# Kernel optimization log

Measured on AMD Instinct MI355X. Metric: run time of the kernel, lower is better.

Reference implementation:

```python
import jax, jax.numpy as jnp
import numpy as np

N_USER, N_ITEM, D = 50000, 30000, 64
N = N_USER + N_ITEM
NNZ_UI, NNZ_R, NNZ_II = 1000000, 800000, 300000
IMG_F, TXT_F = 512, 384
EPS = 1e-5


def spmm(rows, cols, vals, x, n_out):
    # sparse [n_out, n_in] @ dense [n_in, d] via gather + segment-sum
    return jax.ops.segment_sum(vals[:, None] * x[cols], rows, num_segments=n_out)


def leaky_relu(x):
    return jnp.where(x >= 0, x, 0.01 * x)


def setup_inputs() -> dict:
    key = jax.random.key(0)
    ks = jax.random.split(key, 32)
    f = lambda i, shape, s=0.05: (jax.random.normal(ks[i], shape, dtype=jnp.float32) * s)
    inp = {
        'user_emb': f(0, (N_USER, D)),
        'item_emb': f(1, (N_ITEM, D)),
        'image_embedding': f(2, (N_ITEM, IMG_F), 1.0),
        'text_embedding': f(3, (N_ITEM, TXT_F), 1.0),
        'W_img': f(4, (IMG_F, D)), 'b_img': jnp.zeros((D,), jnp.float32),
        'bn_g_img': jnp.ones((D,), jnp.float32), 'bn_b_img': jnp.zeros((D,), jnp.float32),
        'W_txt': f(5, (TXT_F, D)), 'b_txt': jnp.zeros((D,), jnp.float32),
        'bn_g_txt': jnp.ones((D,), jnp.float32), 'bn_b_txt': jnp.zeros((D,), jnp.float32),
        'W_gate_img': f(6, (D, D)), 'b_gate_img': jnp.zeros((D,), jnp.float32),
        'W_gate_txt': f(7, (D, D)), 'b_gate_txt': jnp.zeros((D,), jnp.float32),
        'W_common1': f(8, (D, D)), 'b_common1': jnp.zeros((D,), jnp.float32),
        'w_common2': f(9, (D,)),
        'ui_vals': jax.random.uniform(ks[10], (NNZ_UI,), dtype=jnp.float32),
        'R_vals': jax.random.uniform(ks[11], (NNZ_R,), dtype=jnp.float32),
        'ii_img_vals': jax.random.uniform(ks[12], (NNZ_II,), dtype=jnp.float32),
        'ii_txt_vals': jax.random.uniform(ks[13], (NNZ_II,), dtype=jnp.float32),
        'ui_rows': jax.random.randint(ks[14], (NNZ_UI,), 0, N, dtype=jnp.int32),
        'ui_cols': jax.random.randint(ks[15], (NNZ_UI,), 0, N, dtype=jnp.int32),
        'R_rows': jax.random.randint(ks[16], (NNZ_R,), 0, N_USER, dtype=jnp.int32),
        'R_cols': jax.random.randint(ks[17], (NNZ_R,), 0, N_ITEM, dtype=jnp.int32),
        'ii_img_rows': jax.random.randint(ks[18], (NNZ_II,), 0, N_ITEM, dtype=jnp.int32),
        'ii_img_cols': jax.random.randint(ks[19], (NNZ_II,), 0, N_ITEM, dtype=jnp.int32),
        'ii_txt_rows': jax.random.randint(ks[20], (NNZ_II,), 0, N_ITEM, dtype=jnp.int32),
        'ii_txt_cols': jax.random.randint(ks[21], (NNZ_II,), 0, N_ITEM, dtype=jnp.int32),
    }
    return inp


def reference(user_emb, item_emb, image_embedding, text_embedding,
              W_img, b_img, bn_g_img, bn_b_img,
              W_txt, b_txt, bn_g_txt, bn_b_txt,
              W_gate_img, b_gate_img, W_gate_txt, b_gate_txt,
              W_common1, b_common1, w_common2,
              ui_vals, R_vals, ii_img_vals, ii_txt_vals,
              ui_rows, ui_cols, R_rows, R_cols,
              ii_img_rows, ii_img_cols, ii_txt_rows, ii_txt_cols):
    # ---- user_item_GCN: adj = original + diffusion (fused edge list) ----
    cat = jnp.concatenate([item_emb, user_emb], axis=0)  # [N, D], item first per source
    embs = [cat]
    for _ in range(2):
        cat = spmm(ui_rows, ui_cols, ui_vals, cat, N)
        embs.append(cat)
    content_embedding = jnp.stack(embs, axis=1).mean(axis=1)  # [N, D]

    # ---- modal projections (BN inference, dropout=eval identity) ----
    def project(x, W, b, g, beta):
        h = x @ W + b
        h = h * (g / jnp.sqrt(1.0 + EPS)) + beta  # BatchNorm1d, running stats (0, 1)
        return leaky_relu(h)

    img_feat = project(image_embedding, W_img, b_img, bn_g_img, bn_b_img)  # [I, D]
    txt_feat = project(text_embedding, W_txt, b_txt, bn_g_txt, bn_b_txt)

    # ---- item_item_GCN ----
    def modal_branch(feat, Wg, bg, rows, cols, vals):
        it = item_emb * jax.nn.sigmoid(feat @ Wg + bg)  # gated item embedding
        for _ in range(2):
            it = spmm(rows, cols, vals, it, N_ITEM)
        us = spmm(R_rows, R_cols, R_vals, it, N_USER)  # R @ item -> user
        return jnp.concatenate([us, it], axis=0)  # [N, D], user first per source

    image_ui = modal_branch(img_feat, W_gate_img, b_gate_img, ii_img_rows, ii_img_cols, ii_img_vals)
    text_ui = modal_branch(txt_feat, W_gate_txt, b_gate_txt, ii_txt_rows, ii_txt_cols, ii_txt_vals)

    # ---- gate_attention_fusion (non-tiktok: 2 modalities) ----
    def att_score(e):
        return leaky_relu(e @ W_common1 + b_common1) @ w_common2  # [N]

    att = jnp.stack([att_score(image_ui), att_score(text_ui)], axis=-1)  # [N, 2]
    w = jax.nn.softmax(att, axis=-1)
    common = w[:, 0:1] * image_ui + w[:, 1:2] * text_ui
    special_img = image_ui - common
    special_txt = text_ui - common

    return jnp.stack([content_embedding, special_img, special_txt, common], axis=0)  # [4, N, D]
```

## Files before the change

kernel.cpp:

```cpp
#include <hip/hip_runtime.h>

#define N_USER 50000
#define N_ITEM 30000
#define DIM    64
#define NTOT   80000
#define NNZ_UI 1000000
#define NNZ_R  800000
#define NNZ_II 300000
#define IMG_F  512
#define TXT_F  384

#define NROWS_ALL 190000
#define NNZ_ALL   2400000
#define BASE_R    NTOT
#define BASE_II   (NTOT + N_USER)
#define BASE_IT   (NTOT + N_USER + N_ITEM)

#define RB_BITS   9
#define RB_ROWS   512
#define NBUCK     ((NROWS_ALL + RB_ROWS - 1) / RB_ROWS)
#define NBLK_A2   400
#define EDG_A2    6000

#define NBLK_PG   625
#define NBLK_UIP  5000
#define NBLK_I16  1875
#define NBLK_U16  3125
#define NBLK_CP   1875

#define NBLK_M1   (2 * NBLK_PG + NBLK_UIP)
#define NBLK_M2   (NBLK_UIP + 2 * NBLK_I16)
#define NBLK_RC   (NBLK_U16 + 2 * NBLK_CP)

__device__ __forceinline__ int edge_row(int i,
        const int* __restrict__ r0, const int* __restrict__ r1,
        const int* __restrict__ r2, const int* __restrict__ r3){
    if (i < NNZ_UI)                       return r0[i];
    if (i < NNZ_UI + NNZ_R)               return BASE_R  + r1[i - NNZ_UI];
    if (i < NNZ_UI + NNZ_R + NNZ_II)      return BASE_II + r2[i - NNZ_UI - NNZ_R];
    return BASE_IT + r3[i - NNZ_UI - NNZ_R - NNZ_II];
}

__device__ __forceinline__ void edge_all(int i,
        const int* __restrict__ r0, const int* __restrict__ c0, const float* __restrict__ v0,
        const int* __restrict__ r1, const int* __restrict__ c1, const float* __restrict__ v1,
        const int* __restrict__ r2, const int* __restrict__ c2, const float* __restrict__ v2,
        const int* __restrict__ r3, const int* __restrict__ c3, const float* __restrict__ v3,
        int& gr, int& col, float& val){
    if (i < NNZ_UI){
        gr = r0[i]; col = c0[i]; val = v0[i];
    } else if (i < NNZ_UI + NNZ_R){
        int j = i - NNZ_UI;               gr = BASE_R  + r1[j]; col = c1[j]; val = v1[j];
    } else if (i < NNZ_UI + NNZ_R + NNZ_II){
        int j = i - NNZ_UI - NNZ_R;       gr = BASE_II + r2[j]; col = c2[j]; val = v2[j];
    } else {
        int j = i - NNZ_UI - NNZ_R - NNZ_II; gr = BASE_IT + r3[j]; col = c3[j]; val = v3[j];
    }
}

__global__ __launch_bounds__(256) void k_bhist(const int* __restrict__ r0,
        const int* __restrict__ r1, const int* __restrict__ r2,
        const int* __restrict__ r3, int* __restrict__ bcnt){
    __shared__ int h[NBUCK];
    for (int i = threadIdx.x; i < NBUCK; i += 256) h[i] = 0;
    __syncthreads();
    const int stride = gridDim.x * 256;
    for (int i = blockIdx.x * 256 + threadIdx.x; i < NNZ_ALL; i += stride){
        int gr = edge_row(i, r0, r1, r2, r3);
        atomicAdd(&h[gr >> RB_BITS], 1);
    }
    __syncthreads();
    for (int i = threadIdx.x; i < NBUCK; i += 256){
        int c = h[i];
        if (c) atomicAdd(&bcnt[i], c);
    }
}

__global__ __launch_bounds__(512) void k_bscan(const int* __restrict__ bcnt,
        int* __restrict__ bbase, int* __restrict__ off){
    __shared__ int sh[512];
    const int t = threadIdx.x;
    int v = (t < NBUCK) ? bcnt[t] : 0;
    sh[t] = v;
    __syncthreads();
    for (int d = 1; d < 512; d <<= 1){
        int u = (t >= d) ? sh[t - d] : 0;
        __syncthreads();
        sh[t] += u;
        __syncthreads();
    }
    if (t < NBUCK) bbase[t] = sh[t] - v;
    if (t == NBUCK - 1){
        bbase[NBUCK] = sh[t];
        off[NROWS_ALL] = sh[t];
    }
}

__global__ __launch_bounds__(256) void k_bin(
        const int* __restrict__ r0, const int* __restrict__ c0, const float* __restrict__ v0,
        const int* __restrict__ r1, const int* __restrict__ c1, const float* __restrict__ v1,
        const int* __restrict__ r2, const int* __restrict__ c2, const float* __restrict__ v2,
        const int* __restrict__ r3, const int* __restrict__ c3, const float* __restrict__ v3,
        const int* __restrict__ bbase, int* __restrict__ bcur,
        int2* __restrict__ binned){
    __shared__ int lofs[NBUCK];
    __shared__ int lcur[NBUCK];
    const int t = threadIdx.x;
    for (int i = t; i < NBUCK; i += 256){ lofs[i] = 0; lcur[i] = 0; }
    __syncthreads();
    const int s0 = blockIdx.x * EDG_A2, s1 = s0 + EDG_A2;
    for (int i = s0 + t; i < s1; i += 256){
        int gr = edge_row(i, r0, r1, r2, r3);
        atomicAdd(&lofs[gr >> RB_BITS], 1);
    }
    __syncthreads();
    for (int i = t; i < NBUCK; i += 256){
        int c = lofs[i];
        lofs[i] = c ? (bbase[i] + atomicAdd(&bcur[i], c)) : 0;
    }
    __syncthreads();
    for (int i = s0 + t; i < s1; i += 256){
        int gr, col; float val;
        edge_all(i, r0, c0, v0, r1, c1, v1, r2, c2, v2, r3, c3, v3, gr, col, val);
        int b = gr >> RB_BITS;
        int slot = atomicAdd(&lcur[b], 1);
        binned[lofs[b] + slot] = make_int2((col << RB_BITS) | (gr & (RB_ROWS - 1)),
                                           __float_as_int(val));
    }
}

__global__ __launch_bounds__(256) void k_scatter(const int* __restrict__ bbase,
        const int2* __restrict__ binned, int* __restrict__ off,
        int2* __restrict__ csr){
    __shared__ int h[RB_ROWS];
    const int t = threadIdx.x;
    const int b = blockIdx.x;
    const int base = bbase[b];
    const int nb = bbase[b + 1] - base;
    h[t] = 0; h[t + 256] = 0;
    __syncthreads();
    for (int i = t; i < nb; i += 256)
        atomicAdd(&h[binned[base + i].x & (RB_ROWS - 1)], 1);
    __syncthreads();
    if (t < 64){
        int v[8], s = 0;
#pragma unroll
        for (int k = 0; k < 8; ++k){ v[k] = h[t * 8 + k]; s += v[k]; }
        int incl = s;
#pragma unroll
        for (int d = 1; d < 64; d <<= 1){
            int u = __shfl_up(incl, d, 64);
            if (t >= d) incl += u;
        }
        int run = incl - s;
#pragma unroll
        for (int k = 0; k < 8; ++k){ int tmp = v[k]; h[t * 8 + k] = run; run += tmp; }
    }
    __syncthreads();
    const int row0 = b << RB_BITS;
    for (int i = t; i < RB_ROWS; i += 256){
        int r = row0 + i;
        if (r < NROWS_ALL) off[r] = base + h[i];
    }
    __syncthreads();
    for (int i = t; i < nb; i += 256){
        int2 rec = binned[base + i];
        int lr = rec.x & (RB_ROWS - 1);
        int slot = atomicAdd(&h[lr], 1);
        csr[base + slot] = make_int2(rec.x >> RB_BITS, rec.y);
    }
}

__device__ __forceinline__ const float* cat_row(int c,
        const float* __restrict__ item, const float* __restrict__ user){
    return (c < N_ITEM) ? (item + ((long)c << 6)) : (user + ((long)(c - N_ITEM) << 6));
}

__device__ __forceinline__ void fma4(float4& a, float v, const float4& x){
    a.x = fmaf(v, x.x, a.x);
    a.y = fmaf(v, x.y, a.y);
    a.z = fmaf(v, x.z, a.z);
    a.w = fmaf(v, x.w, a.w);
}

__device__ __forceinline__ void pull_body(const int* __restrict__ off,
        const int2* __restrict__ csr, const float* __restrict__ x,
        float* __restrict__ y, int r, int l){
    int s = off[r], e = off[r + 1];
    float4 a0 = {0.f,0.f,0.f,0.f}, a1 = {0.f,0.f,0.f,0.f};
    float4 a2 = {0.f,0.f,0.f,0.f}, a3 = {0.f,0.f,0.f,0.f};
    int j = s;
    for (; j + 4 <= e; j += 4){
        int2 e0 = csr[j], e1 = csr[j+1], e2 = csr[j+2], e3 = csr[j+3];
        const float4 x0 = *reinterpret_cast<const float4*>(x + ((long)e0.x << 6) + l);
        const float4 x1 = *reinterpret_cast<const float4*>(x + ((long)e1.x << 6) + l);
        const float4 x2 = *reinterpret_cast<const float4*>(x + ((long)e2.x << 6) + l);
        const float4 x3 = *reinterpret_cast<const float4*>(x + ((long)e3.x << 6) + l);
        fma4(a0, __int_as_float(e0.y), x0);
        fma4(a1, __int_as_float(e1.y), x1);
        fma4(a2, __int_as_float(e2.y), x2);
        fma4(a3, __int_as_float(e3.y), x3);
    }
    for (; j < e; ++j){
        int2 e0 = csr[j];
        const float4 x0 = *reinterpret_cast<const float4*>(x + ((long)e0.x << 6) + l);
        fma4(a0, __int_as_float(e0.y), x0);
    }
    a0.x = (a0.x + a1.x) + (a2.x + a3.x);
    a0.y = (a0.y + a1.y) + (a2.y + a3.y);
    a0.z = (a0.z + a1.z) + (a2.z + a3.z);
    a0.w = (a0.w + a1.w) + (a2.w + a3.w);
    *reinterpret_cast<float4*>(y + ((long)r << 6) + l) = a0;
}

__device__ __forceinline__ void pull_cat_body(const int* __restrict__ off,
        const int2* __restrict__ csr, const float* __restrict__ item,
        const float* __restrict__ user, float* __restrict__ y, int r, int l){
    int s = off[r], e = off[r + 1];
    float4 a0 = {0.f,0.f,0.f,0.f}, a1 = {0.f,0.f,0.f,0.f};
    float4 a2 = {0.f,0.f,0.f,0.f}, a3 = {0.f,0.f,0.f,0.f};
    int j = s;
    for (; j + 4 <= e; j += 4){
        int2 e0 = csr[j], e1 = csr[j+1], e2 = csr[j+2], e3 = csr[j+3];
        const float4 x0 = *reinterpret_cast<const float4*>(cat_row(e0.x, item, user) + l);
        const float4 x1 = *reinterpret_cast<const float4*>(cat_row(e1.x, item, user) + l);
        const float4 x2 = *reinterpret_cast<const float4*>(cat_row(e2.x, item, user) + l);
        const float4 x3 = *reinterpret_cast<const float4*>(cat_row(e3.x, item, user) + l);
        fma4(a0, __int_as_float(e0.y), x0);
        fma4(a1, __int_as_float(e1.y), x1);
        fma4(a2, __int_as_float(e2.y), x2);
        fma4(a3, __int_as_float(e3.y), x3);
    }
    for (; j < e; ++j){
        int2 e0 = csr[j];
        const float4 x0 = *reinterpret_cast<const float4*>(cat_row(e0.x, item, user) + l);
        fma4(a0, __int_as_float(e0.y), x0);
    }
    a0.x = (a0.x + a1.x) + (a2.x + a3.x);
    a0.y = (a0.y + a1.y) + (a2.y + a3.y);
    a0.z = (a0.z + a1.z) + (a2.z + a3.z);
    a0.w = (a0.w + a1.w) + (a2.w + a3.w);
    *reinterpret_cast<float4*>(y + ((long)r << 6) + l) = a0;
}

__device__ __forceinline__ void pull_mean_body(const int* __restrict__ off,
        const int2* __restrict__ csr, const float* __restrict__ x,
        const float* __restrict__ item, const float* __restrict__ user,
        float* __restrict__ o0, int r, int l){
    int s = off[r], e = off[r + 1];
    float4 a0 = {0.f,0.f,0.f,0.f}, a1 = {0.f,0.f,0.f,0.f};
    float4 a2 = {0.f,0.f,0.f,0.f}, a3 = {0.f,0.f,0.f,0.f};
    int j = s;
    for (; j + 4 <= e; j += 4){
        int2 e0 = csr[j], e1 = csr[j+1], e2 = csr[j+2], e3 = csr[j+3];
        const float4 x0 = *reinterpret_cast<const float4*>(x + ((long)e0.x << 6) + l);
        const float4 x1 = *reinterpret_cast<const float4*>(x + ((long)e1.x << 6) + l);
        const float4 x2 = *reinterpret_cast<const float4*>(x + ((long)e2.x << 6) + l);
        const float4 x3 = *reinterpret_cast<const float4*>(x + ((long)e3.x << 6) + l);
        fma4(a0, __int_as_float(e0.y), x0);
        fma4(a1, __int_as_float(e1.y), x1);
        fma4(a2, __int_as_float(e2.y), x2);
        fma4(a3, __int_as_float(e3.y), x3);
    }
    for (; j < e; ++j){
        int2 e0 = csr[j];
        const float4 x0 = *reinterpret_cast<const float4*>(x + ((long)e0.x << 6) + l);
        fma4(a0, __int_as_float(e0.y), x0);
    }
    a0.x = (a0.x + a1.x) + (a2.x + a3.x);
    a0.y = (a0.y + a1.y) + (a2.y + a3.y);
    a0.z = (a0.z + a1.z) + (a2.z + a3.z);
    a0.w = (a0.w + a1.w) + (a2.w + a3.w);
    const float4 av = *reinterpret_cast<const float4*>(cat_row(r, item, user) + l);
    const float4 xv = *reinterpret_cast<const float4*>(x + ((long)r << 6) + l);
    float4 o;
    o.x = (av.x + xv.x + a0.x) * (1.0f / 3.0f);
    o.y = (av.y + xv.y + a0.y) * (1.0f / 3.0f);
    o.z = (av.z + xv.z + a0.z) * (1.0f / 3.0f);
    o.w = (av.w + xv.w + a0.w) * (1.0f / 3.0f);
    *reinterpret_cast<float4*>(o0 + ((long)r << 6) + l) = o;
}

__global__ void k_pull2(const int* __restrict__ offA, const int2* __restrict__ csr,
                        const float* __restrict__ xA, float* __restrict__ yA,
                        const int* __restrict__ offB, const float* __restrict__ xB,
                        float* __restrict__ yB, int nrows, int nblk_half){
    int b = blockIdx.x;
    const int* off; const float* x; float* y;
    if (b < nblk_half){ off = offA; x = xA; y = yA; }
    else              { b -= nblk_half; off = offB; x = xB; y = yB; }
    int t = b * 256 + threadIdx.x;
    int r = t >> 4;
    if (r >= nrows) return;
    pull_body(off, csr, x, y, r, (t & 15) << 2);
}

__global__ __launch_bounds__(256) void k_mega1(
        const int* __restrict__ offUI, const int2* __restrict__ csr,
        const float* __restrict__ user,
        float* __restrict__ hop1out,
        const float* __restrict__ Xi, const float* __restrict__ Wi,
        const float* __restrict__ bi, const float* __restrict__ gi,
        const float* __restrict__ bei, const float* __restrict__ Wgi,
        const float* __restrict__ bgi,
        const float* __restrict__ Xt, const float* __restrict__ Wt,
        const float* __restrict__ bt, const float* __restrict__ gt,
        const float* __restrict__ bet, const float* __restrict__ Wgt,
        const float* __restrict__ bgt,
        const float* __restrict__ item,
        float* __restrict__ Pi, float* __restrict__ Pt){
    __shared__ float xs[48][36];
    __shared__ float ws[32][64];

    if (blockIdx.x >= 2 * NBLK_PG){
        int pb = blockIdx.x - 2 * NBLK_PG;
        int t = pb * 256 + threadIdx.x;
        int r = t >> 4;
        pull_cat_body(offUI, csr, item, user, hop1out, r, (t & 15) << 2);
        return;
    }

    const int t  = threadIdx.x;
    const int tr = t >> 4;
    const int tc = t & 15;
    const int pgb = blockIdx.x;
    const bool isTxt = pgb >= NBLK_PG;
    const int  blk   = isTxt ? (pgb - NBLK_PG) : pgb;
    const int  K     = isTxt ? TXT_F : IMG_F;
    const float* X   = isTxt ? Xt  : Xi;
    const float* W   = isTxt ? Wt  : Wi;
    const float* bb  = isTxt ? bt  : bi;
    const float* gg  = isTxt ? gt  : gi;
    const float* be  = isTxt ? bet : bei;
    const float* Wg  = isTxt ? Wgt : Wgi;
    const float* bg  = isTxt ? bgt : bgi;
    float* outP      = isTxt ? Pt  : Pi;
    const int row0   = blk * 48;

    float acc[3][4];
#pragma unroll
    for (int i = 0; i < 3; ++i)
#pragma unroll
        for (int j = 0; j < 4; ++j) acc[i][j] = 0.f;

    for (int ks = 0; ks < K; ks += 32){
        __syncthreads();
        {
            int row = t >> 3, col = (t & 7) << 2;
            *reinterpret_cast<float4*>(&xs[row][col]) =
                *reinterpret_cast<const float4*>(X + (long)(row0 + row) * K + ks + col);
            int f = t + 256;
            if (f < 384){
                row = f >> 3; col = (f & 7) << 2;
                *reinterpret_cast<float4*>(&xs[row][col]) =
                    *reinterpret_cast<const float4*>(X + (long)(row0 + row) * K + ks + col);
            }
        }
        {
            const float4* wsrc = reinterpret_cast<const float4*>(W + (long)ks * 64);
            float4* wdst = reinterpret_cast<float4*>(&ws[0][0]);
            wdst[t]       = wsrc[t];
            wdst[t + 256] = wsrc[t + 256];
        }
        __syncthreads();
#pragma unroll 8
        for (int kk = 0; kk < 32; kk += 2){
            float2 a[3];
#pragma unroll
            for (int i = 0; i < 3; ++i)
                a[i] = *reinterpret_cast<const float2*>(&xs[tr + 16 * i][kk]);
            float4 b0 = *reinterpret_cast<const float4*>(&ws[kk][tc * 4]);
            float4 b1 = *reinterpret_cast<const float4*>(&ws[kk + 1][tc * 4]);
#pragma unroll
            for (int i = 0; i < 3; ++i){
                acc[i][0] = fmaf(a[i].x, b0.x, acc[i][0]);
                acc[i][1] = fmaf(a[i].x, b0.y, acc[i][1]);
                acc[i][2] = fmaf(a[i].x, b0.z, acc[i][2]);
                acc[i][3] = fmaf(a[i].x, b0.w, acc[i][3]);
                acc[i][0] = fmaf(a[i].y, b1.x, acc[i][0]);
                acc[i][1] = fmaf(a[i].y, b1.y, acc[i][1]);
                acc[i][2] = fmaf(a[i].y, b1.z, acc[i][2]);
                acc[i][3] = fmaf(a[i].y, b1.w, acc[i][3]);
            }
        }
    }

    const float4 b4  = reinterpret_cast<const float4*>(bb)[tc];
    const float4 g4  = reinterpret_cast<const float4*>(gg)[tc];
    const float4 be4 = reinterpret_cast<const float4*>(be)[tc];
    float4 h[3];
#pragma unroll
    for (int i = 0; i < 3; ++i){
        h[i].x = (acc[i][0] + b4.x) * (g4.x * 0.99999500003749943f) + be4.x;
        h[i].y = (acc[i][1] + b4.y) * (g4.y * 0.99999500003749943f) + be4.y;
        h[i].z = (acc[i][2] + b4.z) * (g4.z * 0.99999500003749943f) + be4.z;
        h[i].w = (acc[i][3] + b4.w) * (g4.w * 0.99999500003749943f) + be4.w;
        h[i].x = (h[i].x >= 0.f) ? h[i].x : 0.01f * h[i].x;
        h[i].y = (h[i].y >= 0.f) ? h[i].y : 0.01f * h[i].y;
        h[i].z = (h[i].z >= 0.f) ? h[i].z : 0.01f * h[i].z;
        h[i].w = (h[i].w >= 0.f) ? h[i].w : 0.01f * h[i].w;
    }

    float ac2[3][4];
#pragma unroll
    for (int i = 0; i < 3; ++i)
#pragma unroll
        for (int j = 0; j < 4; ++j) ac2[i][j] = 0.f;

#pragma unroll
    for (int ph = 0; ph < 2; ++ph){
        __syncthreads();
        if ((tc >> 3) == ph){
            int lc = (tc & 7) << 2;
#pragma unroll
            for (int i = 0; i < 3; ++i)
                *reinterpret_cast<float4*>(&xs[tr + 16 * i][lc]) = h[i];
        }
        {
            const float4* wsrc = reinterpret_cast<const float4*>(Wg) + ph * 512;
            float4* wdst = reinterpret_cast<float4*>(&ws[0][0]);
            wdst[t]       = wsrc[t];
            wdst[t + 256] = wsrc[t + 256];
        }
        __syncthreads();
#pragma unroll 8
        for (int kk = 0; kk < 32; kk += 2){
            float2 a[3];
#pragma unroll
            for (int i = 0; i < 3; ++i)
                a[i] = *reinterpret_cast<const float2*>(&xs[tr + 16 * i][kk]);
            float4 b0 = *reinterpret_cast<const float4*>(&ws[kk][tc * 4]);
            float4 b1 = *reinterpret_cast<const float4*>(&ws[kk + 1][tc * 4]);
#pragma unroll
            for (int i = 0; i < 3; ++i){
                ac2[i][0] = fmaf(a[i].x, b0.x, ac2[i][0]);
                ac2[i][1] = fmaf(a[i].x, b0.y, ac2[i][1]);
                ac2[i][2] = fmaf(a[i].x, b0.z, ac2[i][2]);
                ac2[i][3] = fmaf(a[i].x, b0.w, ac2[i][3]);
                ac2[i][0] = fmaf(a[i].y, b1.x, ac2[i][0]);
                ac2[i][1] = fmaf(a[i].y, b1.y, ac2[i][1]);
                ac2[i][2] = fmaf(a[i].y, b1.z, ac2[i][2]);
                ac2[i][3] = fmaf(a[i].y, b1.w, ac2[i][3]);
            }
        }
    }

    const float4 bg4 = reinterpret_cast<const float4*>(bg)[tc];
#pragma unroll
    for (int i = 0; i < 3; ++i){
        int r = tr + 16 * i;
        const float4 iv = *reinterpret_cast<const float4*>(
                item + (long)(row0 + r) * 64 + tc * 4);
        float4 o;
        o.x = iv.x / (1.f + __expf(-(ac2[i][0] + bg4.x)));
        o.y = iv.y / (1.f + __expf(-(ac2[i][1] + bg4.y)));
        o.z = iv.z / (1.f + __expf(-(ac2[i][2] + bg4.z)));
        o.w = iv.w / (1.f + __expf(-(ac2[i][3] + bg4.w)));
        *reinterpret_cast<float4*>(outP + (long)(row0 + r) * 64 + tc * 4) = o;
    }
}

__global__ void k_mega2c(const int* __restrict__ offUI, const int2* __restrict__ csr,
        const float* __restrict__ hop1,
        const float* __restrict__ item, const float* __restrict__ user,
        float* __restrict__ o0,
        const int* __restrict__ offI2, const float* __restrict__ P_img,
        float* __restrict__ Q_img,
        const int* __restrict__ offT2, const float* __restrict__ P_txt,
        float* __restrict__ Q_txt){
    const int tid = threadIdx.x;
    if (blockIdx.x < NBLK_UIP){
        int t = blockIdx.x * 256 + tid;
        int r = t >> 4;
        pull_mean_body(offUI, csr, hop1, item, user, o0, r, (t & 15) << 2);
    } else {
        int m = blockIdx.x - NBLK_UIP;
        const int* off; const float* x; float* y;
        if (m < NBLK_I16){ off = offI2; x = P_img; y = Q_img; }
        else             { m -= NBLK_I16; off = offT2; x = P_txt; y = Q_txt; }
        int t = m * 256 + tid;
        int r = t >> 4;
        pull_body(off, csr, x, y, r, (t & 15) << 2);
    }
}

__global__ void k_pullRC(const int* __restrict__ off, const int2* __restrict__ csr,
                         const float* __restrict__ xA, float* __restrict__ yA,
                         const float* __restrict__ xB, float* __restrict__ yB,
                         float* __restrict__ dA, float* __restrict__ dB){
    int bid = blockIdx.x;
    const int tid = threadIdx.x;
    if (bid >= NBLK_U16){
        int c = bid - NBLK_U16;
        const float4* src; float4* dst;
        if (c < NBLK_CP){ src = reinterpret_cast<const float4*>(xA);
                          dst = reinterpret_cast<float4*>(dA); }
        else { c -= NBLK_CP; src = reinterpret_cast<const float4*>(xB);
               dst = reinterpret_cast<float4*>(dB); }
        int i = c * 256 + tid;
        dst[i] = src[i];
        return;
    }
    int t = bid * 256 + tid;
    int r = t >> 4;
    int l = (t & 15) << 2;
    int s = off[r], e = off[r + 1];
    float4 pA0 = {0.f,0.f,0.f,0.f}, pA1 = {0.f,0.f,0.f,0.f};
    float4 pB0 = {0.f,0.f,0.f,0.f}, pB1 = {0.f,0.f,0.f,0.f};
    int j = s;
    for (; j + 2 <= e; j += 2){
        int2 e0 = csr[j];
        int2 e1 = csr[j + 1];
        float v0 = __int_as_float(e0.y);
        float v1 = __int_as_float(e1.y);
        long o0 = ((long)e0.x << 6) + l;
        long o1 = ((long)e1.x << 6) + l;
        const float4 xa0 = *reinterpret_cast<const float4*>(xA + o0);
        const float4 xa1 = *reinterpret_cast<const float4*>(xA + o1);
        const float4 xb0 = *reinterpret_cast<const float4*>(xB + o0);
        const float4 xb1 = *reinterpret_cast<const float4*>(xB + o1);
        fma4(pA0, v0, xa0);
        fma4(pA1, v1, xa1);
        fma4(pB0, v0, xb0);
        fma4(pB1, v1, xb1);
    }
    if (j < e){
        int2 e0 = csr[j];
        float v0 = __int_as_float(e0.y);
        long o0 = ((long)e0.x << 6) + l;
        const float4 xa0 = *reinterpret_cast<const float4*>(xA + o0);
        const float4 xb0 = *reinterpret_cast<const float4*>(xB + o0);
        fma4(pA0, v0, xa0);
        fma4(pB0, v0, xb0);
    }
    pA0.x += pA1.x; pA0.y += pA1.y; pA0.z += pA1.z; pA0.w += pA1.w;
    pB0.x += pB1.x; pB0.y += pB1.y; pB0.z += pB1.z; pB0.w += pB1.w;
    *reinterpret_cast<float4*>(yA + ((long)r << 6) + l) = pA0;
    *reinterpret_cast<float4*>(yB + ((long)r << 6) + l) = pB0;
}

__global__ __launch_bounds__(256) void k_fuse(const float* __restrict__ img,
        const float* __restrict__ txt, const float* __restrict__ W1,
        const float* __restrict__ b1, const float* __restrict__ w2,
        float* __restrict__ out){
    __shared__ float si[64][68];
    __shared__ float st[64][68];
    __shared__ float w1s[64][64];
    const int t  = threadIdx.x;
    const int tr = t >> 4;
    const int tc = t & 15;
    const long row0 = (long)blockIdx.x * 64;

#pragma unroll
    for (int i = 0; i < 4; ++i){
        int r = tr + 16 * i;
        *reinterpret_cast<float4*>(&si[r][tc * 4]) =
            *reinterpret_cast<const float4*>(img + (row0 + r) * 64 + tc * 4);
        *reinterpret_cast<float4*>(&st[r][tc * 4]) =
            *reinterpret_cast<const float4*>(txt + (row0 + r) * 64 + tc * 4);
    }
    {
        const float4* wsrc = reinterpret_cast<const float4*>(W1);
        float4* wdst = reinterpret_cast<float4*>(&w1s[0][0]);
#pragma unroll
        for (int i = 0; i < 4; ++i) wdst[t + 256 * i] = wsrc[t + 256 * i];
    }
    __syncthreads();

    float ai[4][4], at[4][4];
#pragma unroll
    for (int i = 0; i < 4; ++i)
#pragma unroll
        for (int j = 0; j < 4; ++j){ ai[i][j] = 0.f; at[i][j] = 0.f; }

#pragma unroll 8
    for (int kk = 0; kk < 64; kk += 2){
        float4 b0 = *reinterpret_cast<const float4*>(&w1s[kk][tc * 4]);
        float4 b1v = *reinterpret_cast<const float4*>(&w1s[kk + 1][tc * 4]);
#pragma unroll
        for (int i = 0; i < 4; ++i){
            float2 a = *reinterpret_cast<const float2*>(&si[tr + 16 * i][kk]);
            float2 c = *reinterpret_cast<const float2*>(&st[tr + 16 * i][kk]);
            ai[i][0] = fmaf(a.x, b0.x, ai[i][0]);
            ai[i][1] = fmaf(a.x, b0.y, ai[i][1]);
            ai[i][2] = fmaf(a.x, b0.z, ai[i][2]);
            ai[i][3] = fmaf(a.x, b0.w, ai[i][3]);
            ai[i][0] = fmaf(a.y, b1v.x, ai[i][0]);
            ai[i][1] = fmaf(a.y, b1v.y, ai[i][1]);
            ai[i][2] = fmaf(a.y, b1v.z, ai[i][2]);
            ai[i][3] = fmaf(a.y, b1v.w, ai[i][3]);
            at[i][0] = fmaf(c.x, b0.x, at[i][0]);
            at[i][1] = fmaf(c.x, b0.y, at[i][1]);
            at[i][2] = fmaf(c.x, b0.z, at[i][2]);
            at[i][3] = fmaf(c.x, b0.w, at[i][3]);
            at[i][0] = fmaf(c.y, b1v.x, at[i][0]);
            at[i][1] = fmaf(c.y, b1v.y, at[i][1]);
            at[i][2] = fmaf(c.y, b1v.z, at[i][2]);
            at[i][3] = fmaf(c.y, b1v.w, at[i][3]);
        }
    }

    const float4 b14 = reinterpret_cast<const float4*>(b1)[tc];
    const float4 w24 = reinterpret_cast<const float4*>(w2)[tc];
    float pi[4], pt[4];
#pragma unroll
    for (int i = 0; i < 4; ++i){
        float hi0 = ai[i][0] + b14.x; hi0 = (hi0 >= 0.f) ? hi0 : 0.01f * hi0;
        float hi1 = ai[i][1] + b14.y; hi1 = (hi1 >= 0.f) ? hi1 : 0.01f * hi1;
        float hi2 = ai[i][2] + b14.z; hi2 = (hi2 >= 0.f) ? hi2 : 0.01f * hi2;
        float hi3 = ai[i][3] + b14.w; hi3 = (hi3 >= 0.f) ? hi3 : 0.01f * hi3;
        float ht0 = at[i][0] + b14.x; ht0 = (ht0 >= 0.f) ? ht0 : 0.01f * ht0;
        float ht1 = at[i][1] + b14.y; ht1 = (ht1 >= 0.f) ? ht1 : 0.01f * ht1;
        float ht2 = at[i][2] + b14.z; ht2 = (ht2 >= 0.f) ? ht2 : 0.01f * ht2;
        float ht3 = at[i][3] + b14.w; ht3 = (ht3 >= 0.f) ? ht3 : 0.01f * ht3;
        pi[i] = fmaf(hi0, w24.x, fmaf(hi1, w24.y, fmaf(hi2, w24.z, hi3 * w24.w)));
        pt[i] = fmaf(ht0, w24.x, fmaf(ht1, w24.y, fmaf(ht2, w24.z, ht3 * w24.w)));
    }
#pragma unroll
    for (int m = 1; m < 16; m <<= 1){
#pragma unroll
        for (int i = 0; i < 4; ++i){
            pi[i] += __shfl_xor(pi[i], m, 64);
            pt[i] += __shfl_xor(pt[i], m, 64);
        }
    }

    const long NTD = (long)NTOT * DIM;
#pragma unroll
    for (int i = 0; i < 4; ++i){
        int r = tr + 16 * i;
        float mx = fmaxf(pi[i], pt[i]);
        float ei = __expf(pi[i] - mx), et = __expf(pt[i] - mx);
        float inv = 1.f / (ei + et);
        float wi = ei * inv, wt = et * inv;
        const float4 ie = *reinterpret_cast<const float4*>(&si[r][tc * 4]);
        const float4 te = *reinterpret_cast<const float4*>(&st[r][tc * 4]);
        float4 cm, oi, ot;
        cm.x = wi * ie.x + wt * te.x;
        cm.y = wi * ie.y + wt * te.y;
        cm.z = wi * ie.z + wt * te.z;
        cm.w = wi * ie.w + wt * te.w;
        oi.x = ie.x - cm.x; oi.y = ie.y - cm.y; oi.z = ie.z - cm.z; oi.w = ie.w - cm.w;
        ot.x = te.x - cm.x; ot.y = te.y - cm.y; ot.z = te.z - cm.z; ot.w = te.w - cm.w;
        long o = (row0 + r) * 64 + tc * 4;
        *reinterpret_cast<float4*>(out + NTD + o)     = oi;
        *reinterpret_cast<float4*>(out + 2 * NTD + o) = ot;
        *reinterpret_cast<float4*>(out + 3 * NTD + o) = cm;
    }
}

extern "C" void kernel_launch(void* const* d_in, const int* in_sizes, int n_in,
                              void* d_out, int out_size, void* d_ws, size_t ws_size,
                              hipStream_t stream){
    const float* user_emb  = (const float*)d_in[0];
    const float* item_emb  = (const float*)d_in[1];
    const float* image_emb = (const float*)d_in[2];
    const float* text_emb  = (const float*)d_in[3];
    const float* W_img = (const float*)d_in[4];
    const float* b_img = (const float*)d_in[5];
    const float* g_img = (const float*)d_in[6];
    const float* be_img= (const float*)d_in[7];
    const float* W_txt = (const float*)d_in[8];
    const float* b_txt = (const float*)d_in[9];
    const float* g_txt = (const float*)d_in[10];
    const float* be_txt= (const float*)d_in[11];
    const float* W_gi  = (const float*)d_in[12];
    const float* b_gi  = (const float*)d_in[13];
    const float* W_gt  = (const float*)d_in[14];
    const float* b_gt  = (const float*)d_in[15];
    const float* W_c1  = (const float*)d_in[16];
    const float* b_c1  = (const float*)d_in[17];
    const float* w_c2  = (const float*)d_in[18];
    const float* ui_vals = (const float*)d_in[19];
    const float* R_vals  = (const float*)d_in[20];
    const float* ii_iv   = (const float*)d_in[21];
    const float* ii_tv   = (const float*)d_in[22];
    const int* ui_rows = (const int*)d_in[23];
    const int* ui_cols = (const int*)d_in[24];
    const int* R_rows  = (const int*)d_in[25];
    const int* R_cols  = (const int*)d_in[26];
    const int* ii_ir   = (const int*)d_in[27];
    const int* ii_ic   = (const int*)d_in[28];
    const int* ii_tr   = (const int*)d_in[29];
    const int* ii_tc   = (const int*)d_in[30];

    const long ND = (long)NTOT * DIM;
    const long ID = (long)N_ITEM * DIM;
    const long UD = (long)N_USER * DIM;

    float* out = (float*)d_out;
    float* o0 = out;
    float* o1 = out + ND;
    float* o2 = out + 2 * ND;
    float* o3 = out + 3 * ND;

    float* P_img = o3;
    float* P_txt = o3 + ID;
    float* Q_img = o1;
    float* Q_txt = o1 + ID;
    float* H_img = o3;
    float* H_txt = o3 + ID;

    int2* binned = (int2*)o0;

    int2* csr   = (int2*)d_ws;
    int*  off   = (int*)(csr + NNZ_ALL);
    int*  bcnt  = off + NROWS_ALL + 4;
    int*  bcur  = bcnt + NBUCK;
    int*  bbase = bcur + NBUCK;

    hipMemsetAsync(bcnt, 0, 2 * NBUCK * sizeof(int), stream);
    k_bhist<<<512, 256, 0, stream>>>(ui_rows, R_rows, ii_ir, ii_tr, bcnt);
    k_bscan<<<1, 512, 0, stream>>>(bcnt, bbase, off);
    k_bin<<<NBLK_A2, 256, 0, stream>>>(
        ui_rows, ui_cols, ui_vals,  R_rows, R_cols, R_vals,
        ii_ir, ii_ic, ii_iv,        ii_tr, ii_tc, ii_tv,
        bbase, bcur, binned);
    k_scatter<<<NBUCK, 256, 0, stream>>>(bbase, binned, off, csr);

    const int* offUI = off;
    const int* offR  = off + BASE_R;
    const int* offI2 = off + BASE_II;
    const int* offT2 = off + BASE_IT;

    k_mega1<<<NBLK_M1, 256, 0, stream>>>(
        offUI, csr, user_emb, o2,
        image_emb, W_img, b_img, g_img, be_img, W_gi, b_gi,
        text_emb,  W_txt, b_txt, g_txt, be_txt, W_gt, b_gt,
        item_emb, P_img, P_txt);

    k_mega2c<<<NBLK_M2, 256, 0, stream>>>(
        offUI, csr, o2, item_emb, user_emb, o0,
        offI2, P_img, Q_img, offT2, P_txt, Q_txt);

    k_pull2<<<2 * NBLK_I16, 256, 0, stream>>>(
        offI2, csr, Q_img, H_img, offT2, Q_txt, H_txt, N_ITEM, NBLK_I16);

    k_pullRC<<<NBLK_RC, 256, 0, stream>>>(
        offR, csr, H_img, o1, H_txt, o2, o1 + UD, o2 + UD);

    k_fuse<<<NTOT / 64, 256, 0, stream>>>(o1, o2, W_c1, b_c1, w_c2, out);
}
```

Before: 562.5 us.

## Fuse histogram, scan and binning into one cooperative kernel; widen projection K-tile

Merges the bucket histogram, the prefix scan and the binning pass into a single cooperative kernel. It reuses the per-block local histogram that binning already computes, separates the phases with grid-wide syncs, and does the scan with a wavefront shuffle. This removes two kernel launches and a second full read of the row arrays. Separately, the projection GEMM in k_mega1 now uses a 64-wide K tile, and the gate GEMM runs in one 64-deep pass instead of two 32-deep phases, which halves the number of block barriers. The cost is larger shared-memory use per block, which may lower occupancy, plus the overhead of grid sync and a requirement that all 400 blocks be co-resident.

```diff
diff --git a/kernel.cpp b/kernel.cpp
--- a/kernel.cpp
+++ b/kernel.cpp
@@ -1,4 +1,7 @@
 #include <hip/hip_runtime.h>
+#include <hip/hip_cooperative_groups.h>
+
+namespace cg = cooperative_groups;
 
 #define N_USER 50000
 #define N_ITEM 30000
@@ -58,51 +61,13 @@
     }
 }
 
-__global__ __launch_bounds__(256) void k_bhist(const int* __restrict__ r0,
-        const int* __restrict__ r1, const int* __restrict__ r2,
-        const int* __restrict__ r3, int* __restrict__ bcnt){
-    __shared__ int h[NBUCK];
-    for (int i = threadIdx.x; i < NBUCK; i += 256) h[i] = 0;
-    __syncthreads();
-    const int stride = gridDim.x * 256;
-    for (int i = blockIdx.x * 256 + threadIdx.x; i < NNZ_ALL; i += stride){
-        int gr = edge_row(i, r0, r1, r2, r3);
-        atomicAdd(&h[gr >> RB_BITS], 1);
-    }
-    __syncthreads();
-    for (int i = threadIdx.x; i < NBUCK; i += 256){
-        int c = h[i];
-        if (c) atomicAdd(&bcnt[i], c);
-    }
-}
-
-__global__ __launch_bounds__(512) void k_bscan(const int* __restrict__ bcnt,
-        int* __restrict__ bbase, int* __restrict__ off){
-    __shared__ int sh[512];
-    const int t = threadIdx.x;
-    int v = (t < NBUCK) ? bcnt[t] : 0;
-    sh[t] = v;
-    __syncthreads();
-    for (int d = 1; d < 512; d <<= 1){
-        int u = (t >= d) ? sh[t - d] : 0;
-        __syncthreads();
-        sh[t] += u;
-        __syncthreads();
-    }
-    if (t < NBUCK) bbase[t] = sh[t] - v;
-    if (t == NBUCK - 1){
-        bbase[NBUCK] = sh[t];
-        off[NROWS_ALL] = sh[t];
-    }
-}
-
-__global__ __launch_bounds__(256) void k_bin(
+__global__ __launch_bounds__(256) void k_build123(
         const int* __restrict__ r0, const int* __restrict__ c0, const float* __restrict__ v0,
         const int* __restrict__ r1, const int* __restrict__ c1, const float* __restrict__ v1,
         const int* __restrict__ r2, const int* __restrict__ c2, const float* __restrict__ v2,
         const int* __restrict__ r3, const int* __restrict__ c3, const float* __restrict__ v3,
-        const int* __restrict__ bbase, int* __restrict__ bcur,
-        int2* __restrict__ binned){
+        int* __restrict__ bcnt, int* __restrict__ bbase, int* __restrict__ off,
+        int* __restrict__ bcur, int2* __restrict__ binned){
     __shared__ int lofs[NBUCK];
     __shared__ int lcur[NBUCK];
     const int t = threadIdx.x;
@@ -114,6 +79,38 @@
         atomicAdd(&lofs[gr >> RB_BITS], 1);
     }
     __syncthreads();
+    for (int i = t; i < NBUCK; i += 256){
+        int c = lofs[i];
+        if (c) atomicAdd(&bcnt[i], c);
+    }
+    cg::this_grid().sync();
+    if (blockIdx.x == 0 && t < 64){
+        int v[8], s = 0;
+#pragma unroll
+        for (int k = 0; k < 8; ++k){
+            int idx = t * 8 + k;
+            v[k] = (idx < NBUCK) ? bcnt[idx] : 0;
+            s += v[k];
+        }
+        int incl = s;
+#pragma unroll
+        for (int d = 1; d < 64; d <<= 1){
+            int u = __shfl_up(incl, d, 64);
+            if (t >= d) incl += u;
+        }
+        int run = incl - s;
+#pragma unroll
+        for (int k = 0; k < 8; ++k){
+            int idx = t * 8 + k;
+            if (idx < NBUCK) bbase[idx] = run;
+            run += v[k];
+        }
+        if (t == 63){
+            bbase[NBUCK] = run;
+            off[NROWS_ALL] = run;
+        }
+    }
+    cg::this_grid().sync();
     for (int i = t; i < NBUCK; i += 256){
         int c = lofs[i];
         lofs[i] = c ? (bbase[i] + atomicAdd(&bcur[i], c)) : 0;
@@ -309,8 +306,8 @@
         const float* __restrict__ bgt,
         const float* __restrict__ item,
         float* __restrict__ Pi, float* __restrict__ Pt){
-    __shared__ float xs[48][36];
-    __shared__ float ws[32][64];
+    __shared__ float xs[48][68];
+    __shared__ float ws[64][64];
 
     if (blockIdx.x >= 2 * NBLK_PG){
         int pb = blockIdx.x - 2 * NBLK_PG;
@@ -343,28 +340,23 @@
 #pragma unroll
         for (int j = 0; j < 4; ++j) acc[i][j] = 0.f;
 
-    for (int ks = 0; ks < K; ks += 32){
+    for (int ks = 0; ks < K; ks += 64){
         __syncthreads();
-        {
-            int row = t >> 3, col = (t & 7) << 2;
-            *reinterpret_cast<float4*>(&xs[row][col]) =
-                *reinterpret_cast<const float4*>(X + (long)(row0 + row) * K + ks + col);
-            int f = t + 256;
-            if (f < 384){
-                row = f >> 3; col = (f & 7) << 2;
-                *reinterpret_cast<float4*>(&xs[row][col]) =
-                    *reinterpret_cast<const float4*>(X + (long)(row0 + row) * K + ks + col);
-            }
+#pragma unroll
+        for (int i = 0; i < 3; ++i){
+            int r = tr + 16 * i;
+            *reinterpret_cast<float4*>(&xs[r][tc * 4]) =
+                *reinterpret_cast<const float4*>(X + (long)(row0 + r) * K + ks + tc * 4);
         }
         {
             const float4* wsrc = reinterpret_cast<const float4*>(W + (long)ks * 64);
             float4* wdst = reinterpret_cast<float4*>(&ws[0][0]);
-            wdst[t]       = wsrc[t];
-            wdst[t + 256] = wsrc[t + 256];
+#pragma unroll
+            for (int i = 0; i < 4; ++i) wdst[t + 256 * i] = wsrc[t + 256 * i];
         }
         __syncthreads();
 #pragma unroll 8
-        for (int kk = 0; kk < 32; kk += 2){
+        for (int kk = 0; kk < 64; kk += 2){
             float2 a[3];
 #pragma unroll
             for (int i = 0; i < 3; ++i)
@@ -388,60 +380,52 @@
     const float4 b4  = reinterpret_cast<const float4*>(bb)[tc];
     const float4 g4  = reinterpret_cast<const float4*>(gg)[tc];
     const float4 be4 = reinterpret_cast<const float4*>(be)[tc];
-    float4 h[3];
+    __syncthreads();
 #pragma unroll
     for (int i = 0; i < 3; ++i){
-        h[i].x = (acc[i][0] + b4.x) * (g4.x * 0.99999500003749943f) + be4.x;
-        h[i].y = (acc[i][1] + b4.y) * (g4.y * 0.99999500003749943f) + be4.y;
-        h[i].z = (acc[i][2] + b4.z) * (g4.z * 0.99999500003749943f) + be4.z;
-        h[i].w = (acc[i][3] + b4.w) * (g4.w * 0.99999500003749943f) + be4.w;
-        h[i].x = (h[i].x >= 0.f) ? h[i].x : 0.01f * h[i].x;
-        h[i].y = (h[i].y >= 0.f) ? h[i].y : 0.01f * h[i].y;
-        h[i].z = (h[i].z >= 0.f) ? h[i].z : 0.01f * h[i].z;
-        h[i].w = (h[i].w >= 0.f) ? h[i].w : 0.01f * h[i].w;
-    }
+        int r = tr + 16 * i;
+        float4 h;
+        h.x = (acc[i][0] + b4.x) * (g4.x * 0.99999500003749943f) + be4.x;
+        h.y = (acc[i][1] + b4.y) * (g4.y * 0.99999500003749943f) + be4.y;
+        h.z = (acc[i][2] + b4.z) * (g4.z * 0.99999500003749943f) + be4.z;
+        h.w = (acc[i][3] + b4.w) * (g4.w * 0.99999500003749943f) + be4.w;
+        h.x = (h.x >= 0.f) ? h.x : 0.01f * h.x;
+        h.y = (h.y >= 0.f) ? h.y : 0.01f * h.y;
+        h.z = (h.z >= 0.f) ? h.z : 0.01f * h.z;
+        h.w = (h.w >= 0.f) ? h.w : 0.01f * h.w;
+        *reinterpret_cast<float4*>(&xs[r][tc * 4]) = h;
+    }
+    {
+        const float4* wsrc = reinterpret_cast<const float4*>(Wg);
+        float4* wdst = reinterpret_cast<float4*>(&ws[0][0]);
+#pragma unroll
+        for (int i = 0; i < 4; ++i) wdst[t + 256 * i] = wsrc[t + 256 * i];
+    }
+    __syncthreads();
 
     float ac2[3][4];
 #pragma unroll
     for (int i = 0; i < 3; ++i)
 #pragma unroll
         for (int j = 0; j < 4; ++j) ac2[i][j] = 0.f;
-
-#pragma unroll
-    for (int ph = 0; ph < 2; ++ph){
-        __syncthreads();
-        if ((tc >> 3) == ph){
-            int lc = (tc & 7) << 2;
-#pragma unroll
-            for (int i = 0; i < 3; ++i)
-                *reinterpret_cast<float4*>(&xs[tr + 16 * i][lc]) = h[i];
-        }
-        {
-            const float4* wsrc = reinterpret_cast<const float4*>(Wg) + ph * 512;
-            float4* wdst = reinterpret_cast<float4*>(&ws[0][0]);
-            wdst[t]       = wsrc[t];
-            wdst[t + 256] = wsrc[t + 256];
-        }
-        __syncthreads();
 #pragma unroll 8
-        for (int kk = 0; kk < 32; kk += 2){
-            float2 a[3];
-#pragma unroll
-            for (int i = 0; i < 3; ++i)
-                a[i] = *reinterpret_cast<const float2*>(&xs[tr + 16 * i][kk]);
-            float4 b0 = *reinterpret_cast<const float4*>(&ws[kk][tc * 4]);
-            float4 b1 = *reinterpret_cast<const float4*>(&ws[kk + 1][tc * 4]);
-#pragma unroll
-            for (int i = 0; i < 3; ++i){
-                ac2[i][0] = fmaf(a[i].x, b0.x, ac2[i][0]);
-                ac2[i][1] = fmaf(a[i].x, b0.y, ac2[i][1]);
-                ac2[i][2] = fmaf(a[i].x, b0.z, ac2[i][2]);
-                ac2[i][3] = fmaf(a[i].x, b0.w, ac2[i][3]);
-                ac2[i][0] = fmaf(a[i].y, b1.x, ac2[i][0]);
-                ac2[i][1] = fmaf(a[i].y, b1.y, ac2[i][1]);
-                ac2[i][2] = fmaf(a[i].y, b1.z, ac2[i][2]);
-                ac2[i][3] = fmaf(a[i].y, b1.w, ac2[i][3]);
-            }
+    for (int kk = 0; kk < 64; kk += 2){
+        float2 a[3];
+#pragma unroll
+        for (int i = 0; i < 3; ++i)
+            a[i] = *reinterpret_cast<const float2*>(&xs[tr + 16 * i][kk]);
+        float4 b0 = *reinterpret_cast<const float4*>(&ws[kk][tc * 4]);
+        float4 b1 = *reinterpret_cast<const float4*>(&ws[kk + 1][tc * 4]);
+#pragma unroll
+        for (int i = 0; i < 3; ++i){
+            ac2[i][0] = fmaf(a[i].x, b0.x, ac2[i][0]);
+            ac2[i][1] = fmaf(a[i].x, b0.y, ac2[i][1]);
+            ac2[i][2] = fmaf(a[i].x, b0.z, ac2[i][2]);
+            ac2[i][3] = fmaf(a[i].x, b0.w, ac2[i][3]);
+            ac2[i][0] = fmaf(a[i].y, b1.x, ac2[i][0]);
+            ac2[i][1] = fmaf(a[i].y, b1.y, ac2[i][1]);
+            ac2[i][2] = fmaf(a[i].y, b1.z, ac2[i][2]);
+            ac2[i][3] = fmaf(a[i].y, b1.w, ac2[i][3]);
         }
     }
 
@@ -710,12 +694,17 @@
     int*  bbase = bcur + NBUCK;
 
     hipMemsetAsync(bcnt, 0, 2 * NBUCK * sizeof(int), stream);
-    k_bhist<<<512, 256, 0, stream>>>(ui_rows, R_rows, ii_ir, ii_tr, bcnt);
-    k_bscan<<<1, 512, 0, stream>>>(bcnt, bbase, off);
-    k_bin<<<NBLK_A2, 256, 0, stream>>>(
-        ui_rows, ui_cols, ui_vals,  R_rows, R_cols, R_vals,
-        ii_ir, ii_ic, ii_iv,        ii_tr, ii_tc, ii_tv,
-        bbase, bcur, binned);
+    {
+        void* args[] = {
+            (void*)&ui_rows, (void*)&ui_cols, (void*)&ui_vals,
+            (void*)&R_rows,  (void*)&R_cols,  (void*)&R_vals,
+            (void*)&ii_ir,   (void*)&ii_ic,   (void*)&ii_iv,
+            (void*)&ii_tr,   (void*)&ii_tc,   (void*)&ii_tv,
+            (void*)&bcnt, (void*)&bbase, (void*)&off, (void*)&bcur, (void*)&binned
+        };
+        hipLaunchCooperativeKernel(reinterpret_cast<void*>(k_build123),
+                                   dim3(NBLK_A2), dim3(256), args, 0, stream);
+    }
     k_scatter<<<NBUCK, 256, 0, stream>>>(bbase, binned, off, csr);
 
     const int* offUI = off;
```

After: 658.9 us. 1.17x slower.
